# Kernel optimization log

Measured on AMD Instinct MI355X. Metric: run time of the kernel, lower is better.

Reference implementation:

```python
import jax, jax.numpy as jnp
import numpy as np

B, L, N, D = 8, 512, 64, 1024  # batch, seq_len, num_entities, hidden_size


def setup_inputs() -> dict:
    key = jax.random.key(0)
    ks = jax.random.split(key, 18)
    g = lambda i, shape: jax.random.normal(ks[i], shape, dtype=jnp.float32) * 0.02
    inp = {
        "h": jax.random.normal(ks[0], (B, L, D), dtype=jnp.float32),
        "span_idx": jax.random.randint(ks[1], (B, N, 2), 0, L, dtype=jnp.int64),
        # SpanMarkerV0 project_start: Linear(D,2D) -> ReLU -> Linear(2D,D)
        "Ws1": g(2, (D, 2 * D)), "bs1": jnp.zeros((2 * D,), jnp.float32),
        "Ws2": g(3, (2 * D, D)), "bs2": jnp.zeros((D,), jnp.float32),
        # SpanMarkerV0 project_end
        "We1": g(4, (D, 2 * D)), "be1": jnp.zeros((2 * D,), jnp.float32),
        "We2": g(5, (2 * D, D)), "be2": jnp.zeros((D,), jnp.float32),
        # SpanMarkerV0 out_project: Linear(2D, 2D)
        "Wo": g(6, (2 * D, 2 * D)), "bo": jnp.zeros((2 * D,), jnp.float32),
        # relationship_projector: Linear(4D,2D) -> ReLU -> Linear(2D,D)
        "Wr1": g(7, (4 * D, 2 * D)), "br1": jnp.zeros((2 * D,), jnp.float32),
        "Wr2": g(8, (2 * D, D)), "br2": jnp.zeros((D,), jnp.float32),
    }
    return inp


def reference(h, span_idx, Ws1, bs1, Ws2, bs2, We1, be1, We2, be2, Wo, bo,
              Wr1, br1, Wr2, br2):
    # ---- SpanMarkerV0 entity encoder (dropout = identity at inference) ----
    start_proj = jax.nn.relu(h @ Ws1 + bs1) @ Ws2 + bs2  # (B, L, D)
    end_proj = jax.nn.relu(h @ We1 + be1) @ We2 + be2    # (B, L, D)
    bidx = jnp.arange(h.shape[0])[:, None]
    start_rep = start_proj[bidx, span_idx[:, :, 0]]      # (B, N, D)
    end_rep = end_proj[bidx, span_idx[:, :, 1]]          # (B, N, D)
    cat = jax.nn.relu(jnp.concatenate([start_rep, end_rep], axis=-1))
    entity_reps = cat @ Wo + bo                          # (B, N, 2D)

    # ---- pairwise relationship projector ----
    # torch: cat([tile_i, tile_j], -1) @ Wr1  ==  e_i @ Wr1[:2D] + e_j @ Wr1[2D:]
    half = Wr1.shape[0] // 2
    hi = entity_reps @ Wr1[:half]                        # (B, N, 2D)
    hj = entity_reps @ Wr1[half:]                        # (B, N, 2D)
    hidden = jax.nn.relu(hi[:, :, None, :] + hj[:, None, :, :] + br1)  # (B,N,N,2D)
    return hidden @ Wr2 + br2                            # (B, N, N, D)
```

## Files before the change

### kernel.cpp

```cpp
#include <hip/hip_runtime.h>
#include <hip/hip_bf16.h>

constexpr int Lseq = 512;
constexpr int Nsp  = 64;
constexpr int Dm   = 1024;
constexpr int D2   = 2048;

typedef __attribute__((ext_vector_type(8))) short short8;
typedef __attribute__((ext_vector_type(4))) float floatx4;
typedef unsigned short u16;
typedef unsigned int   u32;

__device__ __forceinline__ u32 f2bf(float x) {
    u32 u = __float_as_uint(x);
    return (u + 0x7fffu + ((u >> 16) & 1u)) >> 16;
}
__device__ __forceinline__ float bf2f(u32 hbits) {
    return __uint_as_float(hbits << 16);
}
__device__ __forceinline__ u32 pk2(float x0, float x1) {
    __hip_bfloat162 bb = __float22bfloat162_rn(make_float2(x0, x1));
    u32 r; __builtin_memcpy(&r, &bb, 4); return r;
}

__device__ __forceinline__ int swz_idx(int row, int chunk8) {
    return (row * 32 + chunk8 * 8) ^ (((row >> 1) & 3) << 3);
}

__global__ __launch_bounds__(256)
void gather_split(const float* __restrict__ h, const int* __restrict__ span,
                  u16* __restrict__ g_hi, u16* __restrict__ g_lo)
{
    const int row = blockIdx.x, which = blockIdx.y;
    const int b = row >> 6;
    const int idx = span[row * 2 + which];
    const float4* src = (const float4*)(h + ((size_t)b * Lseq + idx) * Dm);
    float4 v = src[threadIdx.x];
    u32 h01 = pk2(v.x, v.y), h23 = pk2(v.z, v.w);
    u32 l01 = pk2(v.x - bf2f(h01 & 0xffffu), v.y - bf2f(h01 >> 16));
    u32 l23 = pk2(v.z - bf2f(h23 & 0xffffu), v.w - bf2f(h23 >> 16));
    size_t off = ((size_t)which * 512 + row) * Dm + (size_t)threadIdx.x * 4;
    *(uint2*)(g_hi + off) = make_uint2(h01, h23);
    *(uint2*)(g_lo + off) = make_uint2(l01, l23);
}

__global__ __launch_bounds__(256)
void gather_rows(const float* __restrict__ h, const int* __restrict__ span,
                 float* __restrict__ gs, float* __restrict__ ge)
{
    const int row = blockIdx.x, which = blockIdx.y;
    const int b = row >> 6;
    const int idx = span[row * 2 + which];
    const float4* src = (const float4*)(h + ((size_t)b * Lseq + idx) * Dm);
    float4* dst = (float4*)((which ? ge : gs) + (size_t)row * Dm);
    dst[threadIdx.x] = src[threadIdx.x];
}

struct TransJobs {
    const float* src[8];
    u16* dh[8];
    u16* dl[8];
    int K[8], N[8], tiles[8];
};

__global__ __launch_bounds__(256)
void transpose_split(TransJobs J)
{
    __shared__ float T[64][65];
    int b = blockIdx.x, j = 0;
    while (b >= J.tiles[j]) { b -= J.tiles[j]; ++j; }
    const float* src = J.src[j];
    const int K = J.K[j], N = J.N[j];
    const int tk = K >> 6;
    const int k0 = (b % tk) * 64, n0 = (b / tk) * 64;
    const int t = threadIdx.x, c = t & 63, r4 = t >> 6;
#pragma unroll
    for (int s = 0; s < 16; ++s) {
        int r = r4 * 16 + s;
        T[r][c] = src[(size_t)(k0 + r) * N + n0 + c];
    }
    __syncthreads();
    u16* dh = J.dh[j];
    u16* dl = J.dl[j];
#pragma unroll
    for (int s = 0; s < 16; ++s) {
        int n = r4 * 16 + s;
        float v = T[c][n];
        u32 hv = f2bf(v);
        dh[(size_t)(n0 + n) * K + k0 + c] = (u16)hv;
        if (dl) dl[(size_t)(n0 + n) * K + k0 + c] = (u16)f2bf(v - bf2f(hv));
    }
}

struct GemmP {
    const u16 *ah0, *ah1, *al0, *al1;
    const u16 *wh0, *wh1, *wl0, *wl1;
    const float *b0, *b1;
    float *of0, *of1;
    u16 *oh0, *oh1, *ol0, *ol1;
    int K, ldc, coloff1, NT;
};

template<bool RELU, bool BIAS, bool SPLIT_OUT>
__global__ __launch_bounds__(256)
void gemm_split(GemmP P)
{
    __shared__ __align__(16) u16 As_h[2 * 64 * 64];
    __shared__ __align__(16) u16 As_l[2 * 64 * 64];
    __shared__ __align__(16) u16 Bs_h[2 * 64 * 64];
    __shared__ __align__(16) u16 Bs_l[2 * 64 * 64];

    const int tid = threadIdx.x, w = tid >> 6, l = tid & 63;
    const int lr = l & 15, lq = l >> 4;

    const int hb = blockIdx.x;
    const int xcd = hb & 7;
    const int j = hb >> 3;
    const int mb = j & 7;
    const int panel = (j >> 3) * 8 + xcd;
    const int nb = panel % P.NT;
    const int z  = panel / P.NT;

    const int m0 = mb * 64, n0 = nb * 64;
    const int K = P.K;

    const u16* ah = z ? P.ah1 : P.ah0;
    const u16* al = z ? P.al1 : P.al0;
    const u16* wh = z ? P.wh1 : P.wh0;
    const u16* wl = z ? P.wl1 : P.wl0;

    const u16* src; u16* ldst;
    if      (w == 0) { src = ah + (size_t)m0 * K; ldst = As_h; }
    else if (w == 1) { src = al + (size_t)m0 * K; ldst = As_l; }
    else if (w == 2) { src = wh + (size_t)n0 * K; ldst = Bs_h; }
    else             { src = wl + (size_t)n0 * K; ldst = Bs_l; }
    const int schunk = (l & 7) ^ ((l >> 3) & 7);
    const u16* sl = src + (size_t)(l >> 3) * K + (size_t)schunk * 8;

    const int rswz = (lr & 7) << 3;

    floatx4 acc[4];
#pragma unroll
    for (int nt = 0; nt < 4; ++nt) acc[nt] = (floatx4){0.f, 0.f, 0.f, 0.f};

    auto stage = [&](int k0, int buf) {
        u16* ld = ldst + buf * 4096;
#pragma unroll
        for (int i = 0; i < 8; ++i)
            __builtin_amdgcn_global_load_lds(
                (const __attribute__((address_space(1))) u32*)(sl + (size_t)i * 8 * K + k0),
                (__attribute__((address_space(3))) u32*)(ld + i * 512), 16, 0, 0);
    };

    const int nsteps = K >> 6;
    stage(0, 0);
    stage(64, 1);

    for (int t = 0; t < nsteps; ++t) {
        if (t + 1 < nsteps) asm volatile("s_waitcnt vmcnt(8)" ::: "memory");
        else                asm volatile("s_waitcnt vmcnt(0)" ::: "memory");
        __builtin_amdgcn_s_barrier();
        __builtin_amdgcn_sched_barrier(0);

        const int bo = (t & 1) * 4096;
#pragma unroll
        for (int kk = 0; kk < 2; ++kk) {
            const int ar = bo + ((((w * 16 + lr) * 64) + kk * 32 + lq * 8) ^ rswz);
            short8 fah = *(const short8*)&As_h[ar];
            short8 fal = *(const short8*)&As_l[ar];
#pragma unroll
            for (int nt = 0; nt < 4; ++nt) {
                const int brd = bo + ((((nt * 16 + lr) * 64) + kk * 32 + lq * 8) ^ rswz);
                short8 fbh = *(const short8*)&Bs_h[brd];
                short8 fbl = *(const short8*)&Bs_l[brd];
                acc[nt] = __builtin_amdgcn_mfma_f32_16x16x32_bf16(fah, fbh, acc[nt], 0, 0, 0);
                acc[nt] = __builtin_amdgcn_mfma_f32_16x16x32_bf16(fal, fbh, acc[nt], 0, 0, 0);
                acc[nt] = __builtin_amdgcn_mfma_f32_16x16x32_bf16(fah, fbl, acc[nt], 0, 0, 0);
            }
        }
        __builtin_amdgcn_sched_barrier(0);
        __builtin_amdgcn_s_barrier();
        if (t + 2 < nsteps) stage((t + 2) * 64, t & 1);
    }

    const float* bias = z ? P.b1 : P.b0;
    const int colb = n0 + (z ? P.coloff1 : 0);
    float bv[4];
    if (BIAS) {
#pragma unroll
        for (int nt = 0; nt < 4; ++nt) bv[nt] = bias[n0 + nt * 16 + lr];
    }
#pragma unroll
    for (int nt = 0; nt < 4; ++nt) {
#pragma unroll
        for (int r = 0; r < 4; ++r) {
            float x = acc[nt][r];
            if (BIAS) x += bv[nt];
            if (RELU) x = fmaxf(x, 0.f);
            const int m = m0 + w * 16 + lq * 4 + r;
            const size_t oidx = (size_t)m * P.ldc + colb + nt * 16 + lr;
            if (SPLIT_OUT) {
                u16* oh = z ? P.oh1 : P.oh0;
                u16* ol = z ? P.ol1 : P.ol0;
                u32 hv = f2bf(x);
                oh[oidx] = (u16)hv;
                ol[oidx] = (u16)f2bf(x - bf2f(hv));
            } else {
                float* of = z ? P.of1 : P.of0;
                of[oidx] = x;
            }
        }
    }
}

template<bool RELU, bool BIAS>
__global__ __launch_bounds__(256)
void gemm_f32(const float* __restrict__ A, int lda,
              const float* __restrict__ W, int ldw,
              const float* __restrict__ bias,
              float* __restrict__ C, int ldc, int K)
{
    __shared__ float As[16][64];
    __shared__ float Ws[16][64];
    const int tid = threadIdx.x;
    const int tx = tid & 15, ty = tid >> 4;
    const int m0 = blockIdx.x * 64, n0 = blockIdx.y * 64;
    const int la_c = tid & 15, la_r = tid >> 4;
    const int lw_n = tid & 63, lw_k = tid >> 6;
    float acc[4][4] = {};
    for (int k0 = 0; k0 < K; k0 += 16) {
#pragma unroll
        for (int s = 0; s < 4; ++s) {
            int m = la_r + 16 * s;
            As[la_c][m] = A[(size_t)(m0 + m) * lda + k0 + la_c];
        }
#pragma unroll
        for (int s = 0; s < 4; ++s) {
            int k = lw_k + 4 * s;
            Ws[k][lw_n] = W[(size_t)(k0 + k) * ldw + n0 + lw_n];
        }
        __syncthreads();
#pragma unroll
        for (int kk = 0; kk < 16; ++kk) {
            float a4[4], w4[4];
            *(float4*)a4 = *(const float4*)&As[kk][ty * 4];
            *(float4*)w4 = *(const float4*)&Ws[kk][tx * 4];
#pragma unroll
            for (int i = 0; i < 4; ++i)
#pragma unroll
                for (int j = 0; j < 4; ++j)
                    acc[i][j] = fmaf(a4[i], w4[j], acc[i][j]);
        }
        __syncthreads();
    }
#pragma unroll
    for (int i = 0; i < 4; ++i) {
        float4 v; float* vp = (float*)&v;
#pragma unroll
        for (int j = 0; j < 4; ++j) {
            float x = acc[i][j];
            if (BIAS) x += bias[n0 + tx * 4 + j];
            if (RELU) x = fmaxf(x, 0.f);
            vp[j] = x;
        }
        *(float4*)&C[(size_t)(m0 + ty * 4 + i) * ldc + n0 + tx * 4] = v;
    }
}

__global__ __launch_bounds__(512, 4)
void big_mfma(const float* __restrict__ hi, const float* __restrict__ hj,
              const float* __restrict__ br1, const u16* __restrict__ Wt,
              const float* __restrict__ br2, float* __restrict__ out)
{
    __shared__ float hiP[2][D2];
    __shared__ __align__(16) u16 Asb[128 * 32];
    __shared__ __align__(16) u16 Bsb[256 * 32];

    const int tid = threadIdx.x;
    const int p = blockIdx.x, n0 = blockIdx.y * 256;
    const int b = p >> 5, bi0 = p * 2;

    const int rowA = tid >> 2, kq = tid & 3;
    const int selA = rowA >> 6, jA = rowA & 63;
    const float* hjrow = hj + ((size_t)b * 64 + jA) * D2 + kq * 8;
    u16* astore = Asb + swz_idx(rowA, kq);
    const float* hip = hiP[selA] + kq * 8;

    float4 pf0 = *(const float4*)(hjrow);
    float4 pf1 = *(const float4*)(hjrow + 4);

    {
        const float4* h0 = (const float4*)(hi + (size_t)bi0 * D2);
        const float4* h1 = (const float4*)(hi + (size_t)(bi0 + 1) * D2);
        const float4* br = (const float4*)br1;
        float4* d0 = (float4*)hiP[0];
        float4* d1 = (float4*)hiP[1];
        const int v = tid;
        float4 bb = br[v];
        float4 a = h0[v];
        a.x += bb.x; a.y += bb.y; a.z += bb.z; a.w += bb.w;
        d0[v] = a;
        float4 c = h1[v];
        c.x += bb.x; c.y += bb.y; c.z += bb.z; c.w += bb.w;
        d1[v] = c;
    }

    const int w = tid >> 6, l = tid & 63;
    const int wm = w & 1, wn = w >> 1;
    const int lr = l & 15, lq = l >> 4;
    const int rswz = ((lr >> 1) & 3) << 3;

    const int schunk = (l & 3) ^ ((l >> 3) & 3);

    floatx4 acc[4][4];
#pragma unroll
    for (int mt = 0; mt < 4; ++mt)
#pragma unroll
        for (int nt = 0; nt < 4; ++nt)
            acc[mt][nt] = (floatx4){0.f, 0.f, 0.f, 0.f};

    for (int k0 = 0; k0 < D2; k0 += 32) {
        __syncthreads();

#pragma unroll
        for (int c = 0; c < 2; ++c) {
            const u16* g = Wt + (size_t)(n0 + w * 32 + c * 16 + (l >> 2)) * D2
                              + k0 + schunk * 8;
            u16* lp = Bsb + (w * 32 + c * 16) * 32;
            __builtin_amdgcn_global_load_lds(
                (const __attribute__((address_space(1))) u32*)g,
                (__attribute__((address_space(3))) u32*)lp, 16, 0, 0);
        }

        {
            float4 h0 = *(const float4*)(hip + k0);
            float4 h1 = *(const float4*)(hip + k0 + 4);
            u32 u0 = pk2(fmaxf(pf0.x + h0.x, 0.f), fmaxf(pf0.y + h0.y, 0.f));
            u32 u1 = pk2(fmaxf(pf0.z + h0.z, 0.f), fmaxf(pf0.w + h0.w, 0.f));
            u32 u2 = pk2(fmaxf(pf1.x + h1.x, 0.f), fmaxf(pf1.y + h1.y, 0.f));
            u32 u3 = pk2(fmaxf(pf1.z + h1.z, 0.f), fmaxf(pf1.w + h1.w, 0.f));
            *(uint4*)astore = make_uint4(u0, u1, u2, u3);
        }

        __syncthreads();

        if (k0 + 32 < D2) {
            pf0 = *(const float4*)(hjrow + k0 + 32);
            pf1 = *(const float4*)(hjrow + k0 + 36);
        }

        short8 af[4], bfr[4];
#pragma unroll
        for (int mt = 0; mt < 4; ++mt)
            af[mt] = *(const short8*)&Asb[(((wm * 64 + mt * 16 + lr) * 32) + lq * 8) ^ rswz];
#pragma unroll
        for (int nt = 0; nt < 4; ++nt)
            bfr[nt] = *(const short8*)&Bsb[(((wn * 64 + nt * 16 + lr) * 32) + lq * 8) ^ rswz];
        __builtin_amdgcn_s_setprio(1);
#pragma unroll
        for (int mt = 0; mt < 4; ++mt)
#pragma unroll
            for (int nt = 0; nt < 4; ++nt)
                acc[mt][nt] = __builtin_amdgcn_mfma_f32_16x16x32_bf16(
                    af[mt], bfr[nt], acc[mt][nt], 0, 0, 0);
        __builtin_amdgcn_s_setprio(0);
    }

    float bias[4];
#pragma unroll
    for (int nt = 0; nt < 4; ++nt)
        bias[nt] = br2[n0 + wn * 64 + nt * 16 + lr];

#pragma unroll
    for (int mt = 0; mt < 4; ++mt) {
        const int mbase = wm * 64 + mt * 16 + lq * 4;
#pragma unroll
        for (int r = 0; r < 4; ++r) {
            const int mm = mbase + r;
            const int sel = mm >> 6, j = mm & 63;
            float* orow = out + (((size_t)(bi0 + sel) * 64 + j) * Dm) + n0 + wn * 64;
#pragma unroll
            for (int nt = 0; nt < 4; ++nt)
                orow[nt * 16 + lr] = acc[mt][nt][r] + bias[nt];
        }
    }
}

extern "C" void kernel_launch(void* const* d_in, const int* in_sizes, int n_in,
                              void* d_out, int out_size, void* d_ws, size_t ws_size,
                              hipStream_t stream) {
    const float* h    = (const float*)d_in[0];
    const int*   span = (const int*)  d_in[1];
    const float* Ws1  = (const float*)d_in[2];
    const float* bs1  = (const float*)d_in[3];
    const float* Ws2  = (const float*)d_in[4];
    const float* bs2  = (const float*)d_in[5];
    const float* We1  = (const float*)d_in[6];
    const float* be1  = (const float*)d_in[7];
    const float* We2  = (const float*)d_in[8];
    const float* be2  = (const float*)d_in[9];
    const float* Wo   = (const float*)d_in[10];
    const float* bo   = (const float*)d_in[11];
    const float* Wr1  = (const float*)d_in[12];
    const float* br1  = (const float*)d_in[13];
    const float* Wr2  = (const float*)d_in[14];
    const float* br2  = (const float*)d_in[15];
    float* out = (float*)d_out;

    dim3 blk(256);
    const size_t REQUIRED = (size_t)120 << 20;

    if (ws_size >= REQUIRED) {
        char* W = (char*)d_ws;
        size_t off = 0;
        auto alloc = [&](size_t bytes) { char* q = W + off; off += bytes; return q; };

        u16* W1t_h = (u16*)alloc((size_t)2 * 2048 * 1024 * 2);
        u16* W1t_l = (u16*)alloc((size_t)2 * 2048 * 1024 * 2);
        u16* W2t_h = (u16*)alloc((size_t)2 * 1024 * 2048 * 2);
        u16* W2t_l = (u16*)alloc((size_t)2 * 1024 * 2048 * 2);
        u16* Wot_h = (u16*)alloc((size_t)2048 * 2048 * 2);
        u16* Wot_l = (u16*)alloc((size_t)2048 * 2048 * 2);
        u16* Wr1t_h = (u16*)alloc((size_t)2 * 2048 * 2048 * 2);
        u16* Wr1t_l = (u16*)alloc((size_t)2 * 2048 * 2048 * 2);
        u16* Wr2t_h = (u16*)alloc((size_t)1024 * 2048 * 2);
        u16* gs_h  = (u16*)alloc((size_t)2 * 512 * 1024 * 2);
        u16* gs_l  = (u16*)alloc((size_t)2 * 512 * 1024 * 2);
        u16* t1_h  = (u16*)alloc((size_t)2 * 512 * 2048 * 2);
        u16* t1_l  = (u16*)alloc((size_t)2 * 512 * 2048 * 2);
        u16* cat_h = (u16*)alloc((size_t)512 * 2048 * 2);
        u16* cat_l = (u16*)alloc((size_t)512 * 2048 * 2);
        u16* ent_h = (u16*)alloc((size_t)512 * 2048 * 2);
        u16* ent_l = (u16*)alloc((size_t)512 * 2048 * 2);
        float* hif = (float*)alloc((size_t)512 * 2048 * 4);
        float* hjf = (float*)alloc((size_t)512 * 2048 * 4);

        TransJobs J;
        J.src[0] = Ws1;  J.dh[0] = W1t_h;                J.dl[0] = W1t_l;                J.K[0] = 1024; J.N[0] = 2048; J.tiles[0] = 512;
        J.src[1] = We1;  J.dh[1] = W1t_h + 2048 * 1024;  J.dl[1] = W1t_l + 2048 * 1024;  J.K[1] = 1024; J.N[1] = 2048; J.tiles[1] = 512;
        J.src[2] = Ws2;  J.dh[2] = W2t_h;                J.dl[2] = W2t_l;                J.K[2] = 2048; J.N[2] = 1024; J.tiles[2] = 512;
        J.src[3] = We2;  J.dh[3] = W2t_h + 1024 * 2048;  J.dl[3] = W2t_l + 1024 * 2048;  J.K[3] = 2048; J.N[3] = 1024; J.tiles[3] = 512;
        J.src[4] = Wo;   J.dh[4] = Wot_h;                J.dl[4] = Wot_l;                J.K[4] = 2048; J.N[4] = 2048; J.tiles[4] = 1024;
        J.src[5] = Wr1;  J.dh[5] = Wr1t_h;               J.dl[5] = Wr1t_l;               J.K[5] = 2048; J.N[5] = 2048; J.tiles[5] = 1024;
        J.src[6] = Wr1 + (size_t)2048 * 2048;
                         J.dh[6] = Wr1t_h + (size_t)2048 * 2048; J.dl[6] = Wr1t_l + (size_t)2048 * 2048;
                                                                          J.K[6] = 2048; J.N[6] = 2048; J.tiles[6] = 1024;
        J.src[7] = Wr2;  J.dh[7] = Wr2t_h;               J.dl[7] = nullptr;              J.K[7] = 2048; J.N[7] = 1024; J.tiles[7] = 512;
        transpose_split<<<dim3(5632), blk, 0, stream>>>(J);

        gather_split<<<dim3(512, 2), blk, 0, stream>>>(h, span, gs_h, gs_l);

        GemmP p1 = {};
        p1.ah0 = gs_h; p1.ah1 = gs_h + 512 * 1024;
        p1.al0 = gs_l; p1.al1 = gs_l + 512 * 1024;
        p1.wh0 = W1t_h; p1.wh1 = W1t_h + 2048 * 1024;
        p1.wl0 = W1t_l; p1.wl1 = W1t_l + 2048 * 1024;
        p1.b0 = bs1; p1.b1 = be1;
        p1.oh0 = t1_h; p1.oh1 = t1_h + 512 * 2048;
        p1.ol0 = t1_l; p1.ol1 = t1_l + 512 * 2048;
        p1.K = 1024; p1.ldc = 2048; p1.coloff1 = 0; p1.NT = 32;
        gemm_split<true, true, true><<<dim3(512), blk, 0, stream>>>(p1);

        GemmP p2 = {};
        p2.ah0 = t1_h; p2.ah1 = t1_h + 512 * 2048;
        p2.al0 = t1_l; p2.al1 = t1_l + 512 * 2048;
        p2.wh0 = W2t_h; p2.wh1 = W2t_h + 1024 * 2048;
        p2.wl0 = W2t_l; p2.wl1 = W2t_l + 1024 * 2048;
        p2.b0 = bs2; p2.b1 = be2;
        p2.oh0 = cat_h; p2.oh1 = cat_h;
        p2.ol0 = cat_l; p2.ol1 = cat_l;
        p2.K = 2048; p2.ldc = 2048; p2.coloff1 = 1024; p2.NT = 16;
        gemm_split<true, true, true><<<dim3(256), blk, 0, stream>>>(p2);

        GemmP p3 = {};
        p3.ah0 = cat_h; p3.al0 = cat_l;
        p3.wh0 = Wot_h; p3.wl0 = Wot_l;
        p3.b0 = bo;
        p3.oh0 = ent_h; p3.ol0 = ent_l;
        p3.K = 2048; p3.ldc = 2048; p3.coloff1 = 0; p3.NT = 32;
        gemm_split<false, true, true><<<dim3(256), blk, 0, stream>>>(p3);

        GemmP p4 = {};
        p4.ah0 = ent_h; p4.ah1 = ent_h;
        p4.al0 = ent_l; p4.al1 = ent_l;
        p4.wh0 = Wr1t_h; p4.wh1 = Wr1t_h + (size_t)2048 * 2048;
        p4.wl0 = Wr1t_l; p4.wl1 = Wr1t_l + (size_t)2048 * 2048;
        p4.of0 = hif; p4.of1 = hjf;
        p4.K = 2048; p4.ldc = 2048; p4.coloff1 = 0; p4.NT = 32;
        gemm_split<false, false, false><<<dim3(512), blk, 0, stream>>>(p4);

        big_mfma<<<dim3(256, 4), dim3(512), 0, stream>>>(hif, hjf, br1, Wr2t_h, br2, out);
    } else {
        u16* Wt = (u16*)d_ws;
        float* ws  = (float*)((char*)d_ws + (size_t)Dm * D2 * 2);
        float* gs  = ws;
        float* ge  = gs  + 512 * Dm;
        float* t1  = ge  + 512 * Dm;
        float* cat = t1  + 512 * D2;
        float* ent = cat + 512 * D2;
        float* hi  = ent + 512 * D2;
        float* hj  = hi  + 512 * D2;

        TransJobs J = {};
        J.src[0] = Wr2; J.dh[0] = Wt; J.dl[0] = nullptr;
        J.K[0] = 2048; J.N[0] = 1024; J.tiles[0] = 512;
        transpose_split<<<dim3(512), blk, 0, stream>>>(J);

        gather_rows<<<dim3(512, 2), blk, 0, stream>>>(h, span, gs, ge);
        gemm_f32<true,  true><<<dim3(8, 32), blk, 0, stream>>>(gs, Dm, Ws1, D2, bs1, t1, D2, Dm);
        gemm_f32<true,  true><<<dim3(8, 16), blk, 0, stream>>>(t1, D2, Ws2, Dm, bs2, cat, D2, D2);
        gemm_f32<true,  true><<<dim3(8, 32), blk, 0, stream>>>(ge, Dm, We1, D2, be1, t1, D2, Dm);
        gemm_f32<true,  true><<<dim3(8, 16), blk, 0, stream>>>(t1, D2, We2, Dm, be2, cat + Dm, D2, D2);
        gemm_f32<false, true><<<dim3(8, 32), blk, 0, stream>>>(cat, D2, Wo, D2, bo, ent, D2, D2);
        gemm_f32<false, false><<<dim3(8, 32), blk, 0, stream>>>(ent, D2, Wr1, D2, nullptr, hi, D2, D2);
        gemm_f32<false, false><<<dim3(8, 32), blk, 0, stream>>>(ent, D2, Wr1 + (size_t)D2 * D2, D2, nullptr, hj, D2, D2);
        big_mfma<<<dim3(256, 4), dim3(512), 0, stream>>>(hi, hj, br1, Wt, br2, out);
    }
}
```

Before: 473.1 us.

## Add 128x128-tile split-bf16 GEMM with 3-stage pipeline for two projection GEMMs

Adds a new GEMM kernel that computes a 128x128 output tile per block, with each wave holding a 64x64 register tile, a K-step of 32 and a triple-buffered LDS pipeline fed by direct global-to-LDS loads. It replaces the 64x64-tile kernel for the first MLP layer and for the Wr1 hi/hj projections. The larger tiles raise operand reuse and cut redundant global loads. In exchange the grid drops from 512 to 128 blocks, which may leave many of the GPU's compute units idle and lower parallelism.

```diff
diff --git a/kernel.cpp b/kernel.cpp
--- a/kernel.cpp
+++ b/kernel.cpp
@@ -136,7 +136,6 @@
     else             { src = wl + (size_t)n0 * K; ldst = Bs_l; }
     const int schunk = (l & 7) ^ ((l >> 3) & 7);
     const u16* sl = src + (size_t)(l >> 3) * K + (size_t)schunk * 8;
-
     const int rswz = (lr & 7) << 3;
 
     floatx4 acc[4];
@@ -208,6 +207,132 @@
             } else {
                 float* of = z ? P.of1 : P.of0;
                 of[oidx] = x;
+            }
+        }
+    }
+}
+
+template<bool RELU, bool BIAS, bool SPLIT_OUT>
+__global__ __launch_bounds__(256, 1)
+void gemm_split128(GemmP P)
+{
+    __shared__ __align__(16) u16 Ah[3 * 128 * 32];
+    __shared__ __align__(16) u16 Al[3 * 128 * 32];
+    __shared__ __align__(16) u16 Bh[3 * 128 * 32];
+    __shared__ __align__(16) u16 Bl[3 * 128 * 32];
+
+    const int tid = threadIdx.x, w = tid >> 6, l = tid & 63;
+    const int lr = l & 15, lq = l >> 4;
+    const int wm = w & 1, wn = w >> 1;
+
+    const int hb = blockIdx.x;
+    const int xcd = hb & 7;
+    const int j = hb >> 3;
+    const int mb = j & 3;
+    const int pp = (j >> 2) * 8 + xcd;
+    const int nb = pp % P.NT;
+    const int z  = pp / P.NT;
+
+    const int m0 = mb * 128, n0 = nb * 128;
+    const int K = P.K;
+
+    const u16* ah = z ? P.ah1 : P.ah0;
+    const u16* al = z ? P.al1 : P.al0;
+    const u16* wh = z ? P.wh1 : P.wh0;
+    const u16* wl = z ? P.wl1 : P.wl0;
+
+    const u16* src; u16* ldst;
+    if      (w == 0) { src = ah + (size_t)m0 * K; ldst = Ah; }
+    else if (w == 1) { src = al + (size_t)m0 * K; ldst = Al; }
+    else if (w == 2) { src = wh + (size_t)n0 * K; ldst = Bh; }
+    else             { src = wl + (size_t)n0 * K; ldst = Bl; }
+    const int schunk = (l & 3) ^ ((l >> 3) & 3);
+    const u16* sl = src + (size_t)(l >> 2) * K + (size_t)schunk * 8;
+    const int rswz = ((lr >> 1) & 3) << 3;
+
+    floatx4 acc[4][4];
+#pragma unroll
+    for (int mt = 0; mt < 4; ++mt)
+#pragma unroll
+        for (int nt = 0; nt < 4; ++nt)
+            acc[mt][nt] = (floatx4){0.f, 0.f, 0.f, 0.f};
+
+    auto stage = [&](int t) {
+        u16* ld = ldst + (t % 3) * 4096;
+        const int k0 = t * 32;
+#pragma unroll
+        for (int i = 0; i < 8; ++i)
+            __builtin_amdgcn_global_load_lds(
+                (const __attribute__((address_space(1))) u32*)(sl + (size_t)i * 16 * K + k0),
+                (__attribute__((address_space(3))) u32*)(ld + i * 512), 16, 0, 0);
+    };
+
+    const int nsteps = K >> 5;
+    stage(0); stage(1); stage(2);
+
+    for (int t = 0; t < nsteps; ++t) {
+        if (t + 3 <= nsteps)      asm volatile("s_waitcnt vmcnt(16)" ::: "memory");
+        else if (t + 2 == nsteps) asm volatile("s_waitcnt vmcnt(8)" ::: "memory");
+        else                      asm volatile("s_waitcnt vmcnt(0)" ::: "memory");
+        __builtin_amdgcn_s_barrier();
+        __builtin_amdgcn_sched_barrier(0);
+
+        const int bo = (t % 3) * 4096;
+        short8 afh[4], afl[4];
+#pragma unroll
+        for (int mt = 0; mt < 4; ++mt) {
+            const int ar = bo + ((((wm * 64 + mt * 16 + lr) * 32) + lq * 8) ^ rswz);
+            afh[mt] = *(const short8*)&Ah[ar];
+            afl[mt] = *(const short8*)&Al[ar];
+        }
+#pragma unroll
+        for (int nt = 0; nt < 4; ++nt) {
+            const int brd = bo + ((((wn * 64 + nt * 16 + lr) * 32) + lq * 8) ^ rswz);
+            short8 bfh = *(const short8*)&Bh[brd];
+            short8 bfl = *(const short8*)&Bl[brd];
+            __builtin_amdgcn_s_setprio(1);
+#pragma unroll
+            for (int mt = 0; mt < 4; ++mt) {
+                acc[mt][nt] = __builtin_amdgcn_mfma_f32_16x16x32_bf16(afh[mt], bfh, acc[mt][nt], 0, 0, 0);
+                acc[mt][nt] = __builtin_amdgcn_mfma_f32_16x16x32_bf16(afl[mt], bfh, acc[mt][nt], 0, 0, 0);
+                acc[mt][nt] = __builtin_amdgcn_mfma_f32_16x16x32_bf16(afh[mt], bfl, acc[mt][nt], 0, 0, 0);
+            }
+            __builtin_amdgcn_s_setprio(0);
+        }
+        __builtin_amdgcn_sched_barrier(0);
+        __builtin_amdgcn_s_barrier();
+        if (t + 3 < nsteps) stage(t + 3);
+    }
+
+    const float* bias = z ? P.b1 : P.b0;
+    const int colb = n0 + (z ? P.coloff1 : 0);
+    float bv[4];
+    if (BIAS) {
+#pragma unroll
+        for (int nt = 0; nt < 4; ++nt)
+            bv[nt] = bias[n0 + wn * 64 + nt * 16 + lr];
+    }
+#pragma unroll
+    for (int mt = 0; mt < 4; ++mt) {
+#pragma unroll
+        for (int r = 0; r < 4; ++r) {
+            const int m = m0 + wm * 64 + mt * 16 + lq * 4 + r;
+#pragma unroll
+            for (int nt = 0; nt < 4; ++nt) {
+                float x = acc[mt][nt][r];
+                if (BIAS) x += bv[nt];
+                if (RELU) x = fmaxf(x, 0.f);
+                const size_t oidx = (size_t)m * P.ldc + colb + wn * 64 + nt * 16 + lr;
+                if (SPLIT_OUT) {
+                    u16* oh = z ? P.oh1 : P.oh0;
+                    u16* ol = z ? P.ol1 : P.ol0;
+                    u32 hv = f2bf(x);
+                    oh[oidx] = (u16)hv;
+                    ol[oidx] = (u16)f2bf(x - bf2f(hv));
+                } else {
+                    float* of = z ? P.of1 : P.of0;
+                    of[oidx] = x;
+                }
             }
         }
     }
@@ -458,8 +583,8 @@
         p1.b0 = bs1; p1.b1 = be1;
         p1.oh0 = t1_h; p1.oh1 = t1_h + 512 * 2048;
         p1.ol0 = t1_l; p1.ol1 = t1_l + 512 * 2048;
-        p1.K = 1024; p1.ldc = 2048; p1.coloff1 = 0; p1.NT = 32;
-        gemm_split<true, true, true><<<dim3(512), blk, 0, stream>>>(p1);
+        p1.K = 1024; p1.ldc = 2048; p1.coloff1 = 0; p1.NT = 16;
+        gemm_split128<true, true, true><<<dim3(128), blk, 0, stream>>>(p1);
 
         GemmP p2 = {};
         p2.ah0 = t1_h; p2.ah1 = t1_h + 512 * 2048;
@@ -486,8 +611,8 @@
         p4.wh0 = Wr1t_h; p4.wh1 = Wr1t_h + (size_t)2048 * 2048;
         p4.wl0 = Wr1t_l; p4.wl1 = Wr1t_l + (size_t)2048 * 2048;
         p4.of0 = hif; p4.of1 = hjf;
-        p4.K = 2048; p4.ldc = 2048; p4.coloff1 = 0; p4.NT = 32;
-        gemm_split<false, false, false><<<dim3(512), blk, 0, stream>>>(p4);
+        p4.K = 2048; p4.ldc = 2048; p4.coloff1 = 0; p4.NT = 16;
+        gemm_split128<false, false, false><<<dim3(128), blk, 0, stream>>>(p4);
 
         big_mfma<<<dim3(256, 4), dim3(512), 0, stream>>>(hif, hjf, br1, Wr2t_h, br2, out);
     } else {
```

Result: slower. 518.5 us (+9.6%).
